# Kernel optimization log

Measured on AMD Instinct MI355X. Metric: run time of the kernel, lower is better.

Reference implementation:

```python
import jax, jax.numpy as jnp
import numpy as np

O, T = 2000, 6000
DIN, DW, DG, H = 2048, 300, 512, 512
VO, VR, L_EXTRA = 1000, 500, 4


def _mlp2(x, Wa, ba, Wb, bb):
    # two-layer MLP with ReLU after every Linear (sg2im build_mlp, final_nonlinearity=True)
    return jax.nn.relu(jax.nn.relu(x @ Wa + ba) @ Wb + bb)


def _triple_conv(obj_vecs, pred_vecs, s, o, Wa, ba, Wb, bb, W2a, b2a, W2b, b2b, alpha=1.0):
    # gather-by-edge -> edge MLP -> scatter-avg back to nodes (GraphTripleConv, pooling='avg')
    n_obj = obj_vecs.shape[0]
    dout = W2b.shape[1]
    cur = jnp.concatenate([obj_vecs[s], pred_vecs, obj_vecs[o]], axis=1)  # [T, 2*Din+Dp]
    t = _mlp2(cur, Wa, ba, Wb, bb)                                        # [T, 2H+Dout]
    new_s, new_p, new_o = t[:, :H], t[:, H:H + dout], t[:, H + dout:]
    pooled = jnp.zeros((n_obj, H), t.dtype).at[s].add(new_s).at[o].add(new_o)
    cnt = jnp.zeros((n_obj,), t.dtype).at[s].add(1.0).at[o].add(1.0)
    pooled = pooled / jnp.maximum(cnt, 1.0)[:, None]
    new_obj = alpha * _mlp2(pooled, W2a, b2a, W2b, b2b)
    return new_obj, new_p


def setup_inputs() -> dict:
    key = jax.random.key(0)
    ks = jax.random.split(key, 32)
    w = lambda k, sh: (jax.random.normal(k, sh, jnp.float32) * 0.02)
    inp = {
        'obj_embs': jax.random.normal(ks[0], (O, DIN), jnp.float32),
        'obj_nums': O,
        'pred_embs': jax.random.normal(ks[1], (T, DIN), jnp.float32),
        'pred_nums': T,
        'rels': jax.random.randint(ks[2], (T, 3), 0, VR, jnp.int64 if jax.config.read('jax_enable_x64') else jnp.int32),
        'objs': jax.random.randint(ks[3], (O,), 0, VO, jnp.int64 if jax.config.read('jax_enable_x64') else jnp.int32),
        # embedding tables
        'obj_table': jax.random.uniform(ks[4], (VO, DW), jnp.float32, -0.1, 0.1),
        'rel_table': jax.random.uniform(ks[5], (VR, DW), jnp.float32, -0.1, 0.1),
        # fusion layers: Linear(img_dim+word_dim -> img_dim) + relu
        'Wf_obj': w(ks[6], (DIN + DW, DIN)), 'bf_obj': jnp.zeros((DIN,), jnp.float32),
        'Wf_rel': w(ks[7], (DIN + DW, DIN)), 'bf_rel': jnp.zeros((DIN,), jnp.float32),
        # GraphTripleConv layer 1: net1 [3*DIN -> H -> 2H+DG], net2 [H -> H -> DG]
        'W1a': w(ks[8], (3 * DIN, H)), 'b1a': jnp.zeros((H,), jnp.float32),
        'W1b': w(ks[9], (H, 2 * H + DG)), 'b1b': jnp.zeros((2 * H + DG,), jnp.float32),
        'W2a': w(ks[10], (H, H)), 'b2a': jnp.zeros((H,), jnp.float32),
        'W2b': w(ks[11], (H, DG)), 'b2b': jnp.zeros((DG,), jnp.float32),
        # GraphTripleConvNet: 4 more layers, net1 [3*DG -> H -> 2H+DG], net2 [H -> H -> DG]
        'Ws1a': w(ks[12], (L_EXTRA, 3 * DG, H)), 'bs1a': jnp.zeros((L_EXTRA, H), jnp.float32),
        'Ws1b': w(ks[13], (L_EXTRA, H, 2 * H + DG)), 'bs1b': jnp.zeros((L_EXTRA, 2 * H + DG), jnp.float32),
        'Ws2a': w(ks[14], (L_EXTRA, H, H)), 'bs2a': jnp.zeros((L_EXTRA, H), jnp.float32),
        'Ws2b': w(ks[15], (L_EXTRA, H, DG)), 'bs2b': jnp.zeros((L_EXTRA, DG), jnp.float32),
    }
    return inp


def reference(obj_embs, obj_nums, pred_embs, pred_nums, rels, objs,
              obj_table, rel_table, Wf_obj, bf_obj, Wf_rel, bf_rel,
              W1a, b1a, W1b, b1b, W2a, b2a, W2b, b2b,
              Ws1a, bs1a, Ws1b, bs1b, Ws2a, bs2a, Ws2b, bs2b):
    s, p, o = rels[:, 0], rels[:, 1], rels[:, 2]
    # embedding lookup + concatenate-fusion (FusionLayer with relu)
    obj_vecs = jax.nn.relu(jnp.concatenate([obj_embs, obj_table[objs]], axis=1) @ Wf_obj + bf_obj)
    pred_vecs = jax.nn.relu(jnp.concatenate([pred_embs, rel_table[p]], axis=1) @ Wf_rel + bf_rel)
    # first GraphTripleConv (img_dim -> gconv_dim)
    obj_vecs, pred_vecs = _triple_conv(obj_vecs, pred_vecs, s, o,
                                       W1a, b1a, W1b, b1b, W2a, b2a, W2b, b2b)
    # GraphTripleConvNet: 4 more layers (gconv_dim -> gconv_dim)
    for i in range(L_EXTRA):
        obj_vecs, pred_vecs = _triple_conv(obj_vecs, pred_vecs, s, o,
                                           Ws1a[i], bs1a[i], Ws1b[i], bs1b[i],
                                           Ws2a[i], bs2a[i], Ws2b[i], bs2b[i])
    # no_imgnorm=True -> no final l2norm
    return obj_vecs, pred_vecs
```

## Files before the change

kernel.cpp:

```cpp
#include <hip/hip_runtime.h>

#define O_N 2000
#define T_N 6000
#define DIN 2048
#define DW  300
#define DG  512
#define HH_ 512

typedef __attribute__((ext_vector_type(8)))  short short8;
typedef __attribute__((ext_vector_type(16))) float f32x16;
typedef unsigned short u16;

__device__ __forceinline__ float4 ld4(const float* p) { return *(const float4*)p; }

__device__ __forceinline__ u16 rbf(float x) {
    unsigned int u = __float_as_uint(x);
    u += 0x7FFFu + ((u >> 16) & 1u);
    return (u16)(u >> 16);
}
__device__ __forceinline__ float fbf(u16 h) {
    return __uint_as_float((unsigned int)h << 16);
}
__device__ __forceinline__ void split3(float x, short& h, short& m, short& l) {
    u16 a = rbf(x);
    float r = x - fbf(a);
    u16 b = rbf(r);
    r -= fbf(b);
    u16 c = rbf(r);
    h = (short)a; m = (short)b; l = (short)c;
}

template<int BM, int BN>
__global__ __launch_bounds__(256, (BM == 64 ? 4 : 2)) void gemm_mx(
    const u16* __restrict__ Ap, int MpA,
    const u16* __restrict__ Bp, int N, int KC, int M,
    const float* __restrict__ bias, int doRelu,
    float* __restrict__ C, int ldc,
    u16* __restrict__ Op, int MpO,
    const u16* __restrict__ Bp2, float* __restrict__ C2, u16* __restrict__ Op2,
    int nbx)
{
    static_assert(BM == 128 || BM == 64, "BM in {64,128}");
    constexpr int WM = BM / 2, WN = BN / 2;
    constexpr int FI = WM / 32, FJ = WN / 32;
    constexpr int UA = 6 * BM;
    constexpr int UB = 6 * BN;
    constexpr int NI = (UA + UB) / 64;
    constexpr int II = (NI + 3) / 4;
    constexpr int BUF = (BM + BN) * 48;
    __shared__ u16 sm[2 * BUF];

    const int tid = threadIdx.x;
    const int w = tid >> 6, lane = tid & 63;
    const int ln31 = lane & 31, lq = lane >> 5;

    int bx = blockIdx.x;
    const u16* Bpl = Bp; float* Cl = C; u16* Opl = Op;
    if (bx >= nbx) { bx -= nbx; Bpl = Bp2; Cl = C2; Opl = Op2; }
    const int n0 = bx * BN, m0 = blockIdx.y * BM;
    const long psA = (long)KC * MpA * 8;
    const long psB = (long)KC * N * 8;

    const u16* gb[II]; int gstep[II]; int lo[II]; bool gv[II];
#pragma unroll
    for (int ii = 0; ii < II; ii++) {
        int n = w + 4 * ii;
        gv[ii] = n < NI;
        int nn = gv[ii] ? n : 0;
        int u0 = nn * 64;
        bool isA = u0 < UA;
        int uu = isA ? u0 : u0 - UA;
        int dim = isA ? BM : BN;
        int row0 = uu % dim, pq = uu / dim;
        int q = pq & 1, p = pq >> 1;
        const u16* pb = (isA ? Ap : Bpl) + (long)p * (isA ? psA : psB);
        int mp = isA ? MpA : N;
        gb[ii] = pb + ((long)q * mp + (isA ? m0 : n0) + row0 + lane) * 8;
        gstep[ii] = mp * 16;
        lo[ii] = (isA ? (pq * BM + row0) : (6 * BM + pq * BN + row0)) * 8 + lane * 8;
    }

    f32x16 ah[FI][FJ], al[FI][FJ];
#pragma unroll
    for (int fi = 0; fi < FI; fi++)
#pragma unroll
        for (int fj = 0; fj < FJ; fj++)
#pragma unroll
            for (int r = 0; r < 16; r++) { ah[fi][fj][r] = 0.f; al[fi][fj][r] = 0.f; }

    const int T = KC >> 1;
    short8 pf[II];
#pragma unroll
    for (int ii = 0; ii < II; ii++) if (gv[ii]) pf[ii] = *(const short8*)(gb[ii]);
#pragma unroll
    for (int ii = 0; ii < II; ii++) if (gv[ii]) *(short8*)(sm + lo[ii]) = pf[ii];
    __syncthreads();

    for (int t = 0; t < T; t++) {
        const int cb = (t & 1) * BUF, nb2 = ((t + 1) & 1) * BUF;
        const bool more = (t + 1) < T;
        if (more) {
#pragma unroll
            for (int ii = 0; ii < II; ii++)
                if (gv[ii]) pf[ii] = *(const short8*)(gb[ii] + (long)(t + 1) * gstep[ii]);
        }
        const u16* ab = sm + cb;
        const u16* bb = ab + 6 * BM * 8;
        short8 af[FI][3];
#pragma unroll
        for (int fi = 0; fi < FI; fi++)
#pragma unroll
            for (int p = 0; p < 3; p++)
                af[fi][p] = *(const short8*)(ab + ((p * 2 + lq) * BM + (w >> 1) * WM + fi * 32 + ln31) * 8);
#pragma unroll
        for (int fj = 0; fj < FJ; fj++) {
            const int rB = (w & 1) * WN + fj * 32 + ln31;
            short8 bh = *(const short8*)(bb + ((0 * 2 + lq) * BN + rB) * 8);
            short8 bm_ = *(const short8*)(bb + ((1 * 2 + lq) * BN + rB) * 8);
            short8 bl = *(const short8*)(bb + ((2 * 2 + lq) * BN + rB) * 8);
#pragma unroll
            for (int fi = 0; fi < FI; fi++) {
                ah[fi][fj] = __builtin_amdgcn_mfma_f32_32x32x16_bf16(af[fi][0], bh,  ah[fi][fj], 0, 0, 0);
                al[fi][fj] = __builtin_amdgcn_mfma_f32_32x32x16_bf16(af[fi][0], bm_, al[fi][fj], 0, 0, 0);
                al[fi][fj] = __builtin_amdgcn_mfma_f32_32x32x16_bf16(af[fi][1], bh,  al[fi][fj], 0, 0, 0);
                al[fi][fj] = __builtin_amdgcn_mfma_f32_32x32x16_bf16(af[fi][0], bl,  al[fi][fj], 0, 0, 0);
                al[fi][fj] = __builtin_amdgcn_mfma_f32_32x32x16_bf16(af[fi][1], bm_, al[fi][fj], 0, 0, 0);
                al[fi][fj] = __builtin_amdgcn_mfma_f32_32x32x16_bf16(af[fi][2], bh,  al[fi][fj], 0, 0, 0);
            }
        }
        if (more) {
#pragma unroll
            for (int ii = 0; ii < II; ii++)
                if (gv[ii]) *(short8*)(sm + nb2 + lo[ii]) = pf[ii];
        }
        __syncthreads();
    }

    float* bounce = (float*)sm + w * 1184;
    const long psO = (long)N * MpO;
#pragma unroll
    for (int fi = 0; fi < FI; fi++) {
#pragma unroll
        for (int fj = 0; fj < FJ; fj++) {
            const int colBase = n0 + (w & 1) * WN + fj * 32;
            const int rowBase = m0 + (w >> 1) * WM + fi * 32;
            float bv = bias ? bias[colBase + ln31] : 0.f;
            float v[16];
#pragma unroll
            for (int r = 0; r < 16; r++) {
                float x = ah[fi][fj][r] + (al[fi][fj][r] + bv);
                if (doRelu) x = fmaxf(x, 0.f);
                v[r] = x;
            }
            if (Cl) {
#pragma unroll
                for (int r = 0; r < 16; r++) {
                    int row = rowBase + (r & 3) + 8 * (r >> 2) + 4 * lq;
                    if (row < M)
                        Cl[(long)row * ldc + colBase + ln31] = v[r];
                }
            }
            if (Opl) {
#pragma unroll
                for (int r = 0; r < 16; r++)
                    bounce[((r & 3) + 8 * (r >> 2) + 4 * lq) * 36 + ln31] = v[r];
#pragma unroll
                for (int u = 0; u < 2; u++) {
                    int urow = ln31, uc = lq + 2 * u;
                    const float* rp = bounce + urow * 36 + uc * 8;
                    short8 h8, m8, l8;
#pragma unroll
                    for (int j = 0; j < 8; j++) {
                        short a, b, c2; split3(rp[j], a, b, c2);
                        h8[j] = a; m8[j] = b; l8[j] = c2;
                    }
                    long cIdx = (long)((colBase + uc * 8) >> 3);
                    long base = (cIdx * MpO + rowBase + urow) * 8;
                    *(short8*)(Opl + base) = h8;
                    *(short8*)(Opl + psO + base) = m8;
                    *(short8*)(Opl + 2 * psO + base) = l8;
                }
            }
        }
    }
}

__global__ __launch_bounds__(256) void split_b(
    const float* __restrict__ W, int K, int N, int KC,
    u16* __restrict__ Op)
{
    __shared__ float tl[64][65];
    const int tid = threadIdx.x;
    const int n0 = blockIdx.x * 64, k0 = blockIdx.y * 64;
    const long ps = (long)KC * N * 8;
#pragma unroll
    for (int l = 0; l < 4; l++) {
        int k = (tid >> 4) + l * 16;
        int nn = (tid & 15) << 2;
        float4 v = make_float4(0.f, 0.f, 0.f, 0.f);
        if (k0 + k < K) v = ld4(W + (long)(k0 + k) * N + n0 + nn);
        tl[k][nn] = v.x; tl[k][nn + 1] = v.y; tl[k][nn + 2] = v.z; tl[k][nn + 3] = v.w;
    }
    __syncthreads();
#pragma unroll
    for (int l = 0; l < 2; l++) {
        int u = tid + l * 256;
        int n = u & 63, c = u >> 6;
        short8 h8, m8, l8;
#pragma unroll
        for (int j = 0; j < 8; j++) {
            short a, b, c2; split3(tl[c * 8 + j][n], a, b, c2);
            h8[j] = a; m8[j] = b; l8[j] = c2;
        }
        long base = ((long)(k0 / 8 + c) * N + n0 + n) * 8;
        *(short8*)(Op + base) = h8;
        *(short8*)(Op + ps + base) = m8;
        *(short8*)(Op + 2 * ps + base) = l8;
    }
}

__device__ __forceinline__ void store_planes(u16* Op, long ps, long base, const float* x)
{
    short8 h8, m8, l8;
#pragma unroll
    for (int j = 0; j < 8; j++) {
        short a, b, c2; split3(x[j], a, b, c2);
        h8[j] = a; m8[j] = b; l8[j] = c2;
    }
    *(short8*)(Op + base) = h8;
    *(short8*)(Op + ps + base) = m8;
    *(short8*)(Op + 2 * ps + base) = l8;
}

__global__ __launch_bounds__(256) void split_concat_a(
    const float* __restrict__ E, int ldE, int KA,
    const float* __restrict__ Tab, int DWc,
    const int* __restrict__ idx, int idxStride,
    int mBase, int Mvalid, int Mp, int KC,
    u16* __restrict__ Op)
{
    int m = blockIdx.x * 256 + threadIdx.x;
    if (m >= Mp) return;
    int c = blockIdx.y;
    int gm = mBase + m;
    float x[8];
    if (gm >= Mvalid) {
#pragma unroll
        for (int j = 0; j < 8; j++) x[j] = 0.f;
    } else {
        int k0 = c * 8;
        if (k0 + 8 <= KA) {
            float4 a = ld4(E + (long)gm * ldE + k0);
            float4 b = ld4(E + (long)gm * ldE + k0 + 4);
            x[0] = a.x; x[1] = a.y; x[2] = a.z; x[3] = a.w;
            x[4] = b.x; x[5] = b.y; x[6] = b.z; x[7] = b.w;
        } else {
            const float* tr = Tab + (long)idx[(long)gm * idxStride] * DWc;
#pragma unroll
            for (int j = 0; j < 8; j++) {
                int k = k0 + j;
                x[j] = (k < KA) ? E[(long)gm * ldE + k]
                                : ((k - KA) < DWc ? tr[k - KA] : 0.f);
            }
        }
    }
    store_planes(Op, (long)KC * Mp * 8, ((long)c * Mp + m) * 8, x);
}

__global__ __launch_bounds__(256) void edge_planes(
    const float* __restrict__ PPv, const float* __restrict__ P1v,
    const float* __restrict__ P2v, const int* __restrict__ rels,
    const float* __restrict__ b1a, int Mp, u16* __restrict__ Op)
{
    int m = blockIdx.x * 256 + threadIdx.x;
    if (m >= Mp) return;
    int c = blockIdx.y;
    float x[8];
    if (m >= T_N) {
#pragma unroll
        for (int j = 0; j < 8; j++) x[j] = 0.f;
    } else {
        int s = rels[3 * m], o = rels[3 * m + 2];
        const float* pp = PPv + (long)m * HH_ + c * 8;
        const float* p1 = P1v + (long)s * HH_ + c * 8;
        const float* p2 = P2v + (long)o * HH_ + c * 8;
        const float* bb = b1a + c * 8;
#pragma unroll
        for (int j = 0; j < 8; j++)
            x[j] = fmaxf(pp[j] + p1[j] + p2[j] + bb[j], 0.f);
    }
    store_planes(Op, (long)64 * Mp * 8, ((long)c * Mp + m) * 8, x);
}

__global__ __launch_bounds__(256) void pool_planes(
    const float* __restrict__ PO, const int* __restrict__ CNT,
    int Mp, u16* __restrict__ Op)
{
    int m = blockIdx.x * 256 + threadIdx.x;
    if (m >= Mp) return;
    int c = blockIdx.y;
    float x[8];
    if (m >= O_N) {
#pragma unroll
        for (int j = 0; j < 8; j++) x[j] = 0.f;
    } else {
        int cc = CNT[m]; float cf = 1.f / (float)(cc < 1 ? 1 : cc);
#pragma unroll
        for (int j = 0; j < 8; j++) x[j] = PO[(long)m * HH_ + c * 8 + j] * cf;
    }
    store_planes(Op, (long)64 * Mp * 8, ((long)c * Mp + m) * 8, x);
}

__global__ __launch_bounds__(256) void predcopy_planes(
    const float* __restrict__ T2, int Mp, u16* __restrict__ Op)
{
    int m = blockIdx.x * 256 + threadIdx.x;
    if (m >= Mp) return;
    int c = blockIdx.y;
    float x[8];
    if (m >= T_N) {
#pragma unroll
        for (int j = 0; j < 8; j++) x[j] = 0.f;
    } else {
#pragma unroll
        for (int j = 0; j < 8; j++) x[j] = T2[(long)m * 1536 + 512 + c * 8 + j];
    }
    store_planes(Op, (long)64 * Mp * 8, ((long)c * Mp + m) * 8, x);
}

__global__ void predcopy_f32(const float* __restrict__ T2, float* __restrict__ dst)
{
    int i = blockIdx.x * 256 + threadIdx.x;
    if (i >= T_N * HH_ / 4) return;
    int e = i / (HH_ / 4);
    int j = (i % (HH_ / 4)) << 2;
    float4 v = ld4(T2 + (long)e * 1536 + 512 + j);
    *(float4*)(dst + (long)e * HH_ + j) = v;
}

__global__ void count_edges(const int* __restrict__ rels, int* __restrict__ CNT)
{
    int e = blockIdx.x * 256 + threadIdx.x;
    if (e >= T_N) return;
    atomicAdd(CNT + rels[3 * e + 0], 1);
    atomicAdd(CNT + rels[3 * e + 2], 1);
}

__global__ void scatter_pool(const float* __restrict__ T2,
                             const int* __restrict__ rels,
                             float* __restrict__ PO)
{
    int e = blockIdx.x;
    int t = threadIdx.x;
    int s = rels[e * 3 + 0];
    int o = rels[e * 3 + 2];
#pragma unroll
    for (int u = 0; u < 2; u++) {
        int j = t + u * 256;
        unsafeAtomicAdd(PO + (long)s * HH_ + j, T2[(long)e * 1536 + j]);
        unsafeAtomicAdd(PO + (long)o * HH_ + j, T2[(long)e * 1536 + 1024 + j]);
    }
}

template<int BM, int BN>
static inline void GX(hipStream_t st, const u16* Ap, int MpA,
                      const u16* Bp, int N, int KC, int M,
                      const float* bias, int relu_,
                      float* C, int ldc, u16* Op, int MpO,
                      const u16* Bp2, float* C2, u16* Op2)
{
    int nbx = N / BN;
    int pair = (Bp2 != nullptr) ? 2 : 1;
    dim3 g(nbx * pair, MpA / BM), b(256);
    gemm_mx<BM, BN><<<g, b, 0, st>>>(Ap, MpA, Bp, N, KC, M, bias, relu_,
                                     C, ldc, Op, MpO, Bp2, C2, Op2, nbx);
}

static inline void SB(hipStream_t st, const float* W, int K, int N, int KC, u16* Op)
{
    dim3 g(N / 64, KC / 8), b(256);
    split_b<<<g, b, 0, st>>>(W, K, N, KC, Op);
}

extern "C" void kernel_launch(void* const* d_in, const int* in_sizes, int n_in,
                              void* d_out, int out_size, void* d_ws, size_t ws_size,
                              hipStream_t stream)
{
    const float* obj_embs  = (const float*)d_in[0];
    const float* pred_embs = (const float*)d_in[2];
    const int*   rels      = (const int*)d_in[4];
    const int*   objs      = (const int*)d_in[5];
    const float* obj_table = (const float*)d_in[6];
    const float* rel_table = (const float*)d_in[7];
    const float* Wf_obj = (const float*)d_in[8];
    const float* bf_obj = (const float*)d_in[9];
    const float* Wf_rel = (const float*)d_in[10];
    const float* bf_rel = (const float*)d_in[11];
    const float* W1a = (const float*)d_in[12];
    const float* b1a = (const float*)d_in[13];
    const float* W1b = (const float*)d_in[14];
    const float* b1b = (const float*)d_in[15];
    const float* W2a = (const float*)d_in[16];
    const float* b2a = (const float*)d_in[17];
    const float* W2b = (const float*)d_in[18];
    const float* b2b = (const float*)d_in[19];
    const float* Ws1a = (const float*)d_in[20];
    const float* bs1a = (const float*)d_in[21];
    const float* Ws1b = (const float*)d_in[22];
    const float* bs1b = (const float*)d_in[23];
    const float* Ws2a = (const float*)d_in[24];
    const float* bs2a = (const float*)d_in[25];
    const float* Ws2b = (const float*)d_in[26];
    const float* bs2b = (const float*)d_in[27];
    float* out = (float*)d_out;

    unsigned char* B8 = (unsigned char*)d_ws;
    constexpr size_t S1O  = 0;
    constexpr size_t S2O  = 29097984;
    constexpr size_t S3AO = 54263808;
    constexpr size_t ZSZ  = 86507520;
    constexpr size_t T2O  = 0;
    constexpr size_t TTO  = 36864000;
    constexpr size_t PVO  = 55345152;
    constexpr size_t PLO  = 73826304;
    constexpr size_t OVO  = 80117760;
    constexpr size_t S3BO = ZSZ;
    constexpr size_t S3CO = S3BO + 6291456;
    constexpr size_t PPO  = S3CO + 6291456;
    constexpr size_t P1O  = PPO + 12288000;
    constexpr size_t P2O  = P1O + 4096000;
    constexpr size_t CNO  = P2O + 4096000;

    u16* S1  = (u16*)(B8 + S1O);
    u16* S2  = (u16*)(B8 + S2O);
    u16* S3A = (u16*)(B8 + S3AO);
    u16* S3B = (u16*)(B8 + S3BO);
    u16* S3C = (u16*)(B8 + S3CO);
    float* T2 = (float*)(B8 + T2O);
    u16* TTp  = (u16*)(B8 + TTO);
    u16* Hp   = (u16*)(B8 + TTO);
    u16* PVp  = (u16*)(B8 + PVO);
    u16* PLp  = (u16*)(B8 + PLO);
    u16* OVp  = (u16*)(B8 + OVO);
    float* PP = (float*)(B8 + PPO);
    float* P1 = (float*)(B8 + P1O);
    float* P2 = (float*)(B8 + P2O);
    float* PO = P1;
    int* CNT  = (int*)(B8 + CNO);

    hipMemsetAsync(CNT, 0, O_N * sizeof(int), stream);
    hipLaunchKernelGGL(count_edges, dim3((T_N + 255) / 256), dim3(256), 0, stream, rels, CNT);

    SB(stream, Wf_obj, DIN + DW, DIN, 296, S3A);
    {
        dim3 g(8, 296), b(256);
        split_concat_a<<<g, b, 0, stream>>>(obj_embs, DIN, DIN, obj_table, DW,
                                            objs, 1, 0, O_N, 2048, 296, S1);
    }
    GX<64, 64>(stream, S1, 2048, S3A, DIN, 296, O_N, bf_obj, 1,
               nullptr, 0, S2, 2048, nullptr, nullptr, nullptr);
    SB(stream, W1a, DIN, HH_, 256, S3B);
    SB(stream, W1a + (size_t)2 * DIN * HH_, DIN, HH_, 256, S3C);
    GX<64, 64>(stream, S2, 2048, S3B, HH_, 256, O_N, nullptr, 0,
               P1, HH_, nullptr, 0, S3C, P2, nullptr);
    SB(stream, Wf_rel, DIN + DW, DIN, 296, S3A);
    SB(stream, W1a + (size_t)DIN * HH_, DIN, HH_, 256, S3B);
    for (int ch = 0; ch < 3; ch++) {
        int ch0 = ch * 2048;
        int mp  = (ch == 2) ? 1920 : 2048;
        int mv  = (ch == 2) ? 1904 : 2048;
        dim3 g((mp + 255) / 256, 296), b(256);
        split_concat_a<<<g, b, 0, stream>>>(pred_embs, DIN, DIN, rel_table, DW,
                                            rels + 1, 3, ch0, T_N, mp, 296, S1);
        GX<64, 64>(stream, S1, mp, S3A, DIN, 296, mv, bf_rel, 1,
                   nullptr, 0, S2, mp, nullptr, nullptr, nullptr);
        GX<64, 64>(stream, S2, mp, S3B, HH_, 256, mv, nullptr, 0,
                   PP + (size_t)ch0 * HH_, HH_, nullptr, 0,
                   nullptr, nullptr, nullptr);
    }

    for (int L = 0; L < 5; L++) {
        const float* bb1a = (L == 0) ? b1a : (bs1a + (size_t)(L - 1) * HH_);
        const float* w1b  = (L == 0) ? W1b : (Ws1b + (size_t)(L - 1) * HH_ * 1536);
        const float* bb1b = (L == 0) ? b1b : (bs1b + (size_t)(L - 1) * 1536);
        const float* w2a  = (L == 0) ? W2a : (Ws2a + (size_t)(L - 1) * HH_ * HH_);
        const float* bb2a = (L == 0) ? b2a : (bs2a + (size_t)(L - 1) * HH_);
        const float* w2b  = (L == 0) ? W2b : (Ws2b + (size_t)(L - 1) * HH_ * DG);
        const float* bb2b = (L == 0) ? b2b : (bs2b + (size_t)(L - 1) * DG);

        if (L > 0) {
            const float* w1a = Ws1a + (size_t)(L - 1) * 3 * HH_ * HH_;
            SB(stream, w1a, HH_, HH_, 64, S3B);
            SB(stream, w1a + (size_t)2 * HH_ * HH_, HH_, HH_, 64, S3C);
            GX<64, 64>(stream, OVp, 2048, S3B, HH_, 64, O_N, nullptr, 0,
                       P1, HH_, nullptr, 0, S3C, P2, nullptr);
            SB(stream, w1a + (size_t)HH_ * HH_, HH_, HH_, 64, S3B);
            GX<64, 64>(stream, PVp, 6016, S3B, HH_, 64, T_N, nullptr, 0,
                       PP, HH_, nullptr, 0, nullptr, nullptr, nullptr);
        }

        {
            dim3 g(24, 64), b(256);
            edge_planes<<<g, b, 0, stream>>>(PP, P1, P2, rels, bb1a, 6016, TTp);
        }
        SB(stream, w1b, HH_, 1536, 64, S3C);
        GX<128, 64>(stream, TTp, 6016, S3C, 1536, 64, T_N, bb1b, 1,
                    T2, 1536, nullptr, 0, nullptr, nullptr, nullptr);
        hipMemsetAsync(PO, 0, (size_t)O_N * HH_ * sizeof(float), stream);
        hipLaunchKernelGGL(scatter_pool, dim3(T_N), dim3(256), 0, stream, T2, rels, PO);
        {
            dim3 g(8, 64), b(256);
            pool_planes<<<g, b, 0, stream>>>(PO, CNT, 2048, PLp);
        }
        SB(stream, w2a, HH_, HH_, 64, S3B);
        GX<64, 64>(stream, PLp, 2048, S3B, HH_, 64, O_N, bb2a, 1,
                   nullptr, 0, Hp, 2048, nullptr, nullptr, nullptr);
        SB(stream, w2b, HH_, DG, 64, S3C);
        if (L < 4) {
            GX<64, 64>(stream, Hp, 2048, S3C, DG, 64, O_N, bb2b, 1,
                       nullptr, 0, OVp, 2048, nullptr, nullptr, nullptr);
            dim3 g(24, 64), b(256);
            predcopy_planes<<<g, b, 0, stream>>>(T2, 6016, PVp);
        } else {
            GX<64, 64>(stream, Hp, 2048, S3C, DG, 64, O_N, bb2b, 1,
                       out, DG, nullptr, 0, nullptr, nullptr, nullptr);
            hipLaunchKernelGGL(predcopy_f32, dim3((T_N * HH_ / 4 + 255) / 256),
                               dim3(256), 0, stream, T2, out + (size_t)O_N * DG);
        }
    }
}
```

Before: 2.151 ms.

## Add intra-block split-K GEMM path with 128x128 tiles for fusion layers

Adds a KS template variant of the bf16x3 MFMA GEMM that launches 512 threads as two 4-wave groups. Each group handles half of the K range in its own double-buffered LDS region, and the partial accumulators are reduced through shared memory before the epilogue. The large K=2348 fusion GEMMs now use 128x128 tiles with this split-K path, and the edge-MLP second GEMM grows from 128x64 to 128x128 tiles. The goal is more data reuse per tile while keeping enough waves active; the cost is more LDS, higher register pressure and fewer blocks per CU.

```diff
diff --git a/kernel.cpp b/kernel.cpp
--- a/kernel.cpp
+++ b/kernel.cpp
@@ -30,8 +30,9 @@
     h = (short)a; m = (short)b; l = (short)c;
 }
 
-template<int BM, int BN>
-__global__ __launch_bounds__(256, (BM == 64 ? 4 : 2)) void gemm_mx(
+template<int BM, int BN, int KS>
+__global__ __launch_bounds__(KS ? 512 : 256, KS ? 2 : (BM == 64 ? 4 : 2))
+void gemm_mx(
     const u16* __restrict__ Ap, int MpA,
     const u16* __restrict__ Bp, int N, int KC, int M,
     const float* __restrict__ bias, int doRelu,
@@ -43,15 +44,18 @@
     static_assert(BM == 128 || BM == 64, "BM in {64,128}");
     constexpr int WM = BM / 2, WN = BN / 2;
     constexpr int FI = WM / 32, FJ = WN / 32;
+    static_assert(!KS || FI == 2, "KS path needs FI=2");
     constexpr int UA = 6 * BM;
     constexpr int UB = 6 * BN;
     constexpr int NI = (UA + UB) / 64;
     constexpr int II = (NI + 3) / 4;
     constexpr int BUF = (BM + BN) * 48;
-    __shared__ u16 sm[2 * BUF];
+    __shared__ u16 sm[(KS ? 4 : 2) * BUF];
 
     const int tid = threadIdx.x;
     const int w = tid >> 6, lane = tid & 63;
+    const int wg = w & 3;
+    const int g = KS ? (w >> 2) : 0;
     const int ln31 = lane & 31, lq = lane >> 5;
 
     int bx = blockIdx.x;
@@ -61,10 +65,16 @@
     const long psA = (long)KC * MpA * 8;
     const long psB = (long)KC * N * 8;
 
+    int c0 = 0, cn = KC;
+    if (KS) { int h = (KC >> 2) << 1; c0 = g ? h : 0; cn = g ? (KC - h) : h; }
+    const u16* ApG = Ap + (long)c0 * MpA * 8;
+    const u16* BpG = Bpl + (long)c0 * N * 8;
+    u16* smg = sm + g * 2 * BUF;
+
     const u16* gb[II]; int gstep[II]; int lo[II]; bool gv[II];
 #pragma unroll
     for (int ii = 0; ii < II; ii++) {
-        int n = w + 4 * ii;
+        int n = wg + 4 * ii;
         gv[ii] = n < NI;
         int nn = gv[ii] ? n : 0;
         int u0 = nn * 64;
@@ -73,7 +83,7 @@
         int dim = isA ? BM : BN;
         int row0 = uu % dim, pq = uu / dim;
         int q = pq & 1, p = pq >> 1;
-        const u16* pb = (isA ? Ap : Bpl) + (long)p * (isA ? psA : psB);
+        const u16* pb = (isA ? ApG : BpG) + (long)p * (isA ? psA : psB);
         int mp = isA ? MpA : N;
         gb[ii] = pb + ((long)q * mp + (isA ? m0 : n0) + row0 + lane) * 8;
         gstep[ii] = mp * 16;
@@ -88,12 +98,12 @@
 #pragma unroll
             for (int r = 0; r < 16; r++) { ah[fi][fj][r] = 0.f; al[fi][fj][r] = 0.f; }
 
-    const int T = KC >> 1;
+    const int T = cn >> 1;
     short8 pf[II];
 #pragma unroll
     for (int ii = 0; ii < II; ii++) if (gv[ii]) pf[ii] = *(const short8*)(gb[ii]);
 #pragma unroll
-    for (int ii = 0; ii < II; ii++) if (gv[ii]) *(short8*)(sm + lo[ii]) = pf[ii];
+    for (int ii = 0; ii < II; ii++) if (gv[ii]) *(short8*)(smg + lo[ii]) = pf[ii];
     __syncthreads();
 
     for (int t = 0; t < T; t++) {
@@ -104,17 +114,17 @@
             for (int ii = 0; ii < II; ii++)
                 if (gv[ii]) pf[ii] = *(const short8*)(gb[ii] + (long)(t + 1) * gstep[ii]);
         }
-        const u16* ab = sm + cb;
+        const u16* ab = smg + cb;
         const u16* bb = ab + 6 * BM * 8;
         short8 af[FI][3];
 #pragma unroll
         for (int fi = 0; fi < FI; fi++)
 #pragma unroll
             for (int p = 0; p < 3; p++)
-                af[fi][p] = *(const short8*)(ab + ((p * 2 + lq) * BM + (w >> 1) * WM + fi * 32 + ln31) * 8);
+                af[fi][p] = *(const short8*)(ab + ((p * 2 + lq) * BM + (wg >> 1) * WM + fi * 32 + ln31) * 8);
 #pragma unroll
         for (int fj = 0; fj < FJ; fj++) {
-            const int rB = (w & 1) * WN + fj * 32 + ln31;
+            const int rB = (wg & 1) * WN + fj * 32 + ln31;
             short8 bh = *(const short8*)(bb + ((0 * 2 + lq) * BN + rB) * 8);
             short8 bm_ = *(const short8*)(bb + ((1 * 2 + lq) * BN + rB) * 8);
             short8 bl = *(const short8*)(bb + ((2 * 2 + lq) * BN + rB) * 8);
@@ -131,7 +141,43 @@
         if (more) {
 #pragma unroll
             for (int ii = 0; ii < II; ii++)
-                if (gv[ii]) *(short8*)(sm + nb2 + lo[ii]) = pf[ii];
+                if (gv[ii]) *(short8*)(smg + nb2 + lo[ii]) = pf[ii];
+        }
+        __syncthreads();
+    }
+
+    float tv[FJ][16];
+    if (KS) {
+        constexpr int XW = FJ * 16 * 64;
+        float* xs = (float*)sm;
+        float* wrp = xs + (1 - g) * 4 * XW + wg * XW;
+        if (g == 0) {
+#pragma unroll
+            for (int fj = 0; fj < FJ; fj++)
+#pragma unroll
+                for (int r = 0; r < 16; r++)
+                    wrp[(fj * 16 + r) * 64 + lane] = ah[1][fj][r] + al[1][fj][r];
+        } else {
+#pragma unroll
+            for (int fj = 0; fj < FJ; fj++)
+#pragma unroll
+                for (int r = 0; r < 16; r++)
+                    wrp[(fj * 16 + r) * 64 + lane] = ah[0][fj][r] + al[0][fj][r];
+        }
+        __syncthreads();
+        float* rdp = xs + g * 4 * XW + wg * XW;
+        if (g == 0) {
+#pragma unroll
+            for (int fj = 0; fj < FJ; fj++)
+#pragma unroll
+                for (int r = 0; r < 16; r++)
+                    tv[fj][r] = ah[0][fj][r] + al[0][fj][r] + rdp[(fj * 16 + r) * 64 + lane];
+        } else {
+#pragma unroll
+            for (int fj = 0; fj < FJ; fj++)
+#pragma unroll
+                for (int r = 0; r < 16; r++)
+                    tv[fj][r] = ah[1][fj][r] + al[1][fj][r] + rdp[(fj * 16 + r) * 64 + lane];
         }
         __syncthreads();
     }
@@ -140,15 +186,17 @@
     const long psO = (long)N * MpO;
 #pragma unroll
     for (int fi = 0; fi < FI; fi++) {
+        if (KS && fi != g) continue;
 #pragma unroll
         for (int fj = 0; fj < FJ; fj++) {
-            const int colBase = n0 + (w & 1) * WN + fj * 32;
-            const int rowBase = m0 + (w >> 1) * WM + fi * 32;
+            const int colBase = n0 + (wg & 1) * WN + fj * 32;
+            const int rowBase = m0 + (wg >> 1) * WM + fi * 32;
             float bv = bias ? bias[colBase + ln31] : 0.f;
             float v[16];
 #pragma unroll
             for (int r = 0; r < 16; r++) {
-                float x = ah[fi][fj][r] + (al[fi][fj][r] + bv);
+                float s = KS ? tv[fj][r] : (ah[fi][fj][r] + al[fi][fj][r]);
+                float x = s + bv;
                 if (doRelu) x = fmaxf(x, 0.f);
                 v[r] = x;
             }
@@ -372,8 +420,20 @@
     int nbx = N / BN;
     int pair = (Bp2 != nullptr) ? 2 : 1;
     dim3 g(nbx * pair, MpA / BM), b(256);
-    gemm_mx<BM, BN><<<g, b, 0, st>>>(Ap, MpA, Bp, N, KC, M, bias, relu_,
-                                     C, ldc, Op, MpO, Bp2, C2, Op2, nbx);
+    gemm_mx<BM, BN, 0><<<g, b, 0, st>>>(Ap, MpA, Bp, N, KC, M, bias, relu_,
+                                        C, ldc, Op, MpO, Bp2, C2, Op2, nbx);
+}
+
+template<int BM, int BN>
+static inline void GK2(hipStream_t st, const u16* Ap, int MpA,
+                       const u16* Bp, int N, int KC, int M,
+                       const float* bias, int relu_,
+                       float* C, int ldc, u16* Op, int MpO)
+{
+    dim3 g(N / BN, MpA / BM), b(512);
+    gemm_mx<BM, BN, 1><<<g, b, 0, st>>>(Ap, MpA, Bp, N, KC, M, bias, relu_,
+                                        C, ldc, Op, MpO,
+                                        nullptr, nullptr, nullptr, N / BN);
 }
 
 static inline void SB(hipStream_t st, const float* W, int K, int N, int KC, u16* Op)
@@ -457,8 +517,8 @@
         split_concat_a<<<g, b, 0, stream>>>(obj_embs, DIN, DIN, obj_table, DW,
                                             objs, 1, 0, O_N, 2048, 296, S1);
     }
-    GX<64, 64>(stream, S1, 2048, S3A, DIN, 296, O_N, bf_obj, 1,
-               nullptr, 0, S2, 2048, nullptr, nullptr, nullptr);
+    GK2<128, 128>(stream, S1, 2048, S3A, DIN, 296, O_N, bf_obj, 1,
+                  nullptr, 0, S2, 2048);
     SB(stream, W1a, DIN, HH_, 256, S3B);
     SB(stream, W1a + (size_t)2 * DIN * HH_, DIN, HH_, 256, S3C);
     GX<64, 64>(stream, S2, 2048, S3B, HH_, 256, O_N, nullptr, 0,
@@ -472,8 +532,8 @@
         dim3 g((mp + 255) / 256, 296), b(256);
         split_concat_a<<<g, b, 0, stream>>>(pred_embs, DIN, DIN, rel_table, DW,
                                             rels + 1, 3, ch0, T_N, mp, 296, S1);
-        GX<64, 64>(stream, S1, mp, S3A, DIN, 296, mv, bf_rel, 1,
-                   nullptr, 0, S2, mp, nullptr, nullptr, nullptr);
+        GK2<128, 128>(stream, S1, mp, S3A, DIN, 296, mv, bf_rel, 1,
+                      nullptr, 0, S2, mp);
         GX<64, 64>(stream, S2, mp, S3B, HH_, 256, mv, nullptr, 0,
                    PP + (size_t)ch0 * HH_, HH_, nullptr, 0,
                    nullptr, nullptr, nullptr);
@@ -504,8 +564,8 @@
             edge_planes<<<g, b, 0, stream>>>(PP, P1, P2, rels, bb1a, 6016, TTp);
         }
         SB(stream, w1b, HH_, 1536, 64, S3C);
-        GX<128, 64>(stream, TTp, 6016, S3C, 1536, 64, T_N, bb1b, 1,
-                    T2, 1536, nullptr, 0, nullptr, nullptr, nullptr);
+        GX<128, 128>(stream, TTp, 6016, S3C, 1536, 64, T_N, bb1b, 1,
+                     T2, 1536, nullptr, 0, nullptr, nullptr, nullptr);
         hipMemsetAsync(PO, 0, (size_t)O_N * HH_ * sizeof(float), stream);
         hipLaunchKernelGGL(scatter_pool, dim3(T_N), dim3(256), 0, stream, T2, rels, PO);
         {
```

After: 2.108 ms. 2.0% less time.
